# Optimization experiments

Measured on AMD Instinct MI355X. Metric: run time of the kernel, lower is better.

Reference implementation:

```python
import jax, jax.numpy as jnp
import numpy as np

N = 170000          # n_users + n_entities
NNZ = 2720000       # edges in sparse A_in (avg degree 16)
DIMS = [64, 64, 32, 16]
NEG_SLOPE = 0.01    # nn.LeakyReLU default
EPS = 1e-12         # F.normalize eps


def setup_inputs() -> dict:
    key = jax.random.key(0)
    ks = jax.random.split(key, 20)
    inp = {
        "embeddings": jax.random.normal(ks[0], (N, DIMS[0]), jnp.float32) * 0.1,
        "a_vals": jax.random.uniform(ks[1], (NNZ,), jnp.float32) / 16.0,  # ~row-normalized
    }
    # bi-interaction layer params, stored (in, out) so y = x @ W + b
    i = 2
    for l in range(3):
        din, dout = DIMS[l], DIMS[l + 1]
        s = 1.0 / np.sqrt(din)
        inp[f"w1_{l}"] = jax.random.normal(ks[i], (din, dout), jnp.float32) * s; i += 1
        inp[f"b1_{l}"] = jnp.zeros((dout,), jnp.float32)
        inp[f"w2_{l}"] = jax.random.normal(ks[i], (din, dout), jnp.float32) * s; i += 1
        inp[f"b2_{l}"] = jnp.zeros((dout,), jnp.float32)
    inp["a_rows"] = jax.random.randint(ks[i], (NNZ,), 0, N, jnp.int32); i += 1
    inp["a_cols"] = jax.random.randint(ks[i], (NNZ,), 0, N, jnp.int32)
    return inp


def _leaky(x):
    return jnp.where(x >= 0, x, NEG_SLOPE * x)


def _l2norm(x):
    n = jnp.sqrt(jnp.sum(x * x, axis=1, keepdims=True))
    return x / jnp.maximum(n, EPS)


def _spmm(vals, rows, cols, emb):
    # sparse A (COO) @ emb : gather source rows, scale, scatter-add to dest rows
    msgs = vals[:, None] * emb[cols]          # (nnz, d)
    return jax.ops.segment_sum(msgs, rows, num_segments=N)


def reference(embeddings, a_vals,
              w1_0, b1_0, w2_0, b2_0,
              w1_1, b1_1, w2_1, b2_1,
              w1_2, b1_2, w2_2, b2_2,
              a_rows, a_cols):
    layers = [(w1_0, b1_0, w2_0, b2_0),
              (w1_1, b1_1, w2_1, b2_1),
              (w1_2, b1_2, w2_2, b2_2)]
    ego = embeddings
    all_embed = [ego]
    for (w1, b1, w2, b2) in layers:
        side = _spmm(a_vals, a_rows, a_cols, ego)            # (N, d_in)
        sum_e = _leaky((ego + side) @ w1 + b1)               # bi-interaction
        bi_e = _leaky((ego * side) @ w2 + b2)
        ego = sum_e + bi_e                                   # dropout = identity (eval)
        all_embed.append(_l2norm(ego))
    return jnp.concatenate(all_embed, axis=1)                # (N, 176)
```

## Files before the change

### kernel.cpp

```cpp
#include <hip/hip_runtime.h>
#include <hip/hip_bf16.h>

#define NEG_SLOPE 0.01f
#define L2EPS 1e-12f
#define SCAN_CHUNK 2048
#define PART_CH 8192
#define BSHIFT 9

__device__ __forceinline__ unsigned short f2bf(float f) {
    unsigned u = __float_as_uint(f);
    return (unsigned short)((u + 0x7fffu + ((u >> 16) & 1u)) >> 16);
}


__global__ void scan_sum(const int* __restrict__ counts, int* __restrict__ partials, int n) {
    __shared__ int red[256];
    int base = blockIdx.x * SCAN_CHUNK;
    int s = 0;
    for (int i = threadIdx.x; i < SCAN_CHUNK; i += 256) {
        int idx = base + i;
        s += (idx < n) ? counts[idx] : 0;
    }
    red[threadIdx.x] = s; __syncthreads();
    for (int o = 128; o > 0; o >>= 1) {
        if (threadIdx.x < o) red[threadIdx.x] += red[threadIdx.x + o];
        __syncthreads();
    }
    if (threadIdx.x == 0) partials[blockIdx.x] = red[0];
}

__global__ void scan_partials(int* __restrict__ partials, int nb, int* __restrict__ out, int n) {
    if (threadIdx.x == 0 && blockIdx.x == 0) {
        int run = 0;
        for (int i = 0; i < nb; i++) { int v = partials[i]; partials[i] = run; run += v; }
        out[n] = run;
    }
}

__global__ void scan_apply(const int* __restrict__ counts, const int* __restrict__ partials,
                           int* __restrict__ out, int n) {
    __shared__ int lsum[256];
    int base = blockIdx.x * SCAN_CHUNK;
    int t = threadIdx.x;
    int my[8];
    int s = 0;
    int tb = base + t * 8;
    for (int i = 0; i < 8; i++) { int idx = tb + i; int v = (idx < n) ? counts[idx] : 0; my[i] = v; s += v; }
    lsum[t] = s; __syncthreads();
    for (int o = 1; o < 256; o <<= 1) {
        int v = (t >= o) ? lsum[t - o] : 0;
        __syncthreads();
        lsum[t] += v;
        __syncthreads();
    }
    int excl = lsum[t] - s + partials[blockIdx.x];
    for (int i = 0; i < 8; i++) {
        int idx = tb + i;
        if (idx < n) { out[idx] = excl; excl += my[i]; }
    }
}


__global__ void part_hist(const int* __restrict__ rows, int* __restrict__ hist,
                          int nnz, int nchunks, int B) {
    __shared__ int h[512];
    int c = blockIdx.x;
    for (int i = threadIdx.x; i < B; i += 256) h[i] = 0;
    __syncthreads();
    int s = c * PART_CH, e = min(s + PART_CH, nnz);
    for (int i = s + threadIdx.x; i < e; i += 256) atomicAdd(&h[rows[i] >> BSHIFT], 1);
    __syncthreads();
    for (int b = threadIdx.x; b < B; b += 256) hist[b * nchunks + c] = h[b];
}

__global__ void part_scatter(const int* __restrict__ rows, const int* __restrict__ cols,
                             const float* __restrict__ vals, const int* __restrict__ hscan,
                             int2* __restrict__ tmp, int nnz, int nchunks, int B) {
    __shared__ int cur[512];
    int c = blockIdx.x;
    for (int b = threadIdx.x; b < B; b += 256) cur[b] = hscan[b * nchunks + c];
    __syncthreads();
    int s = c * PART_CH, e = min(s + PART_CH, nnz);
    for (int i = s + threadIdx.x; i < e; i += 256) {
        int r = rows[i];
        int p = atomicAdd(&cur[r >> BSHIFT], 1);
        unsigned u14 = __float2uint_rn(vals[i] * 262144.0f);
        if (u14 > 16383u) u14 = 16383u;
        tmp[p] = make_int2(((r & 511) << 18) | cols[i], (int)u14);
    }
}

__global__ void bucket_scatter(const int* __restrict__ hscan, const int2* __restrict__ tmp,
                               unsigned* __restrict__ pedge, int* __restrict__ offsets,
                               int nnz, int nchunks, int B, int n) {
    __shared__ int cnt[512];
    __shared__ int scn[256];
    int b = blockIdx.x;
    int t = threadIdx.x;
    int rbase = b << BSHIFT;
    cnt[t] = 0; cnt[t + 256] = 0;
    __syncthreads();
    int s = hscan[b * nchunks];
    int e = (b == B - 1) ? nnz : hscan[(b + 1) * nchunks];
    for (int j = s + t; j < e; j += 256) atomicAdd(&cnt[((unsigned)tmp[j].x) >> 18], 1);
    __syncthreads();
    int c0 = cnt[2 * t], c1 = cnt[2 * t + 1];
    int ssum = c0 + c1;
    scn[t] = ssum;
    __syncthreads();
    for (int o = 1; o < 256; o <<= 1) {
        int v = (t >= o) ? scn[t - o] : 0;
        __syncthreads();
        scn[t] += v;
        __syncthreads();
    }
    int excl = scn[t] - ssum + s;
    int g0 = rbase + 2 * t, g1 = g0 + 1;
    if (g0 < n) offsets[g0] = excl;
    if (g1 < n) offsets[g1] = excl + c0;
    cnt[2 * t] = excl;
    cnt[2 * t + 1] = excl + c0;
    if (b == B - 1 && t == 0) offsets[n] = nnz;
    __syncthreads();
    for (int j = s + t; j < e; j += 256) {
        int2 tt = tmp[j];
        int r9 = ((unsigned)tt.x) >> 18;
        int p = atomicAdd(&cnt[r9], 1);
        pedge[p] = (unsigned)(tt.x & 0x3FFFF) | ((unsigned)tt.y << 18);
    }
}


__global__ void embed_prep(const float* __restrict__ emb, unsigned short* __restrict__ egob,
                           float* __restrict__ outp, int nrows) {
    int idx = blockIdx.x * blockDim.x + threadIdx.x;
    if (idx >= nrows * 16) return;
    int row = idx >> 4, c = idx & 15;
    float4 v = ((const float4*)emb)[idx];
    ((float4*)(outp + (size_t)row * 176))[c] = v;
    ushort4 o;
    o.x = f2bf(v.x); o.y = f2bf(v.y); o.z = f2bf(v.z); o.w = f2bf(v.w);
    ((ushort4*)egob)[idx] = o;
}


__device__ __forceinline__ float leaky1(float x) { return x >= 0.f ? x : NEG_SLOPE * x; }

__device__ __forceinline__ void fma8(float v, uint4 qv, float* acc) {
    acc[0] += v * __uint_as_float(qv.x << 16);
    acc[1] += v * __uint_as_float(qv.x & 0xffff0000u);
    acc[2] += v * __uint_as_float(qv.y << 16);
    acc[3] += v * __uint_as_float(qv.y & 0xffff0000u);
    acc[4] += v * __uint_as_float(qv.z << 16);
    acc[5] += v * __uint_as_float(qv.z & 0xffff0000u);
    acc[6] += v * __uint_as_float(qv.w << 16);
    acc[7] += v * __uint_as_float(qv.w & 0xffff0000u);
}

__device__ __forceinline__ void unpack8(uint4 qv, float* e) {
    e[0] = __uint_as_float(qv.x << 16); e[1] = __uint_as_float(qv.x & 0xffff0000u);
    e[2] = __uint_as_float(qv.y << 16); e[3] = __uint_as_float(qv.y & 0xffff0000u);
    e[4] = __uint_as_float(qv.z << 16); e[5] = __uint_as_float(qv.z & 0xffff0000u);
    e[6] = __uint_as_float(qv.w << 16); e[7] = __uint_as_float(qv.w & 0xffff0000u);
}

#define V14 3.814697265625e-06f

template <int DIN, int DOUT>
__global__ __launch_bounds__(256, 4)
void fused_layer(const unsigned short* __restrict__ egob, const int* __restrict__ offs,
                 const unsigned* __restrict__ pedge,
                 const float* __restrict__ w1, const float* __restrict__ b1,
                 const float* __restrict__ w2, const float* __restrict__ b2,
                 unsigned short* __restrict__ egob_next,
                 float* __restrict__ outp, int col_off, int nrows) {
    constexpr int RPB = 64;
    constexpr int CPL = DIN / 4;
    constexpr int U4  = CPL / 8;
    constexpr int TX  = DOUT / 4;
    constexpr int TY  = 256 / TX;
    constexpr int RPT = RPB / TY;

    __shared__ float sU[DIN][RPB];
    __shared__ float sV[DIN][RPB];

    int tid = threadIdx.x;
    int row0 = blockIdx.x * RPB;

    if (tid < 64) {
        int g = row0 + tid;
        unsigned deg = (g < nrows) ? (unsigned)(offs[g + 1] - offs[g]) : 0u;
        unsigned key = (deg << 6) | (unsigned)tid;
#pragma unroll
        for (int size = 2; size <= 64; size <<= 1) {
#pragma unroll
            for (int stride = size >> 1; stride > 0; stride >>= 1) {
                unsigned other = __shfl_xor(key, stride, 64);
                bool dir = ((tid & size) == 0);
                bool lower = ((tid & stride) == 0);
                bool takeMin = (lower == dir);
                key = takeMin ? (key < other ? key : other) : (key > other ? key : other);
            }
        }
        ((int*)sU)[tid] = (int)(key & 63u);
    }
    __syncthreads();
    int r = tid >> 2, q = tid & 3;
    int pr = ((int*)sU)[r];
    __syncthreads();

    {
        int g = row0 + pr;
        float acc[CPL];
#pragma unroll
        for (int i = 0; i < CPL; i++) acc[i] = 0.f;
        if (g < nrows) {
            int j0 = offs[g], j1 = offs[g + 1];
            uint4 eq[U4];
            const uint4* ep = (const uint4*)(egob + (size_t)g * DIN) + q * U4;
#pragma unroll
            for (int u = 0; u < U4; u++) eq[u] = ep[u];

            int j = j0;
            unsigned ed[4];
            bool have = (j + 4 <= j1);
            if (have) {
#pragma unroll
                for (int m = 0; m < 4; m++) ed[m] = pedge[j + m];
            }
            while (have) {
                uint4 t[4][U4];
#pragma unroll
                for (int m = 0; m < 4; m++) {
                    const uint4* s = (const uint4*)(egob + (size_t)(ed[m] & 0x3FFFFu) * DIN) + q * U4;
#pragma unroll
                    for (int u = 0; u < U4; u++) t[m][u] = s[u];
                }
                bool nxt = (j + 8 <= j1);
                unsigned ed2[4];
                if (nxt) {
#pragma unroll
                    for (int m = 0; m < 4; m++) ed2[m] = pedge[j + 4 + m];
                }
#pragma unroll
                for (int m = 0; m < 4; m++) {
                    float v = (float)(ed[m] >> 18) * V14;
#pragma unroll
                    for (int u = 0; u < U4; u++) fma8(v, t[m][u], acc + u * 8);
                }
#pragma unroll
                for (int m = 0; m < 4; m++) ed[m] = ed2[m];
                j += 4;
                have = nxt;
            }
            for (; j < j1; ++j) {
                unsigned e0 = pedge[j];
                float v0 = (float)(e0 >> 18) * V14;
                const uint4* s0 = (const uint4*)(egob + (size_t)(e0 & 0x3FFFFu) * DIN) + q * U4;
                uint4 qa[U4];
#pragma unroll
                for (int u = 0; u < U4; u++) qa[u] = s0[u];
#pragma unroll
                for (int u = 0; u < U4; u++) fma8(v0, qa[u], acc + u * 8);
            }
#pragma unroll
            for (int u = 0; u < U4; u++) {
                float ev[8];
                unpack8(eq[u], ev);
                int k0 = q * CPL + u * 8;
#pragma unroll
                for (int z = 0; z < 8; z++) {
                    float e = ev[z], a = acc[u * 8 + z];
                    sU[k0 + z][pr] = e + a;
                    sV[k0 + z][pr] = e * a;
                }
            }
        } else {
#pragma unroll
            for (int i = 0; i < CPL; i++) { sU[q * CPL + i][pr] = 0.f; sV[q * CPL + i][pr] = 0.f; }
        }
    }
    __syncthreads();

    int tx = tid % TX, ty = tid / TX;
    float4 a1[RPT], a2[RPT];
#pragma unroll
    for (int i = 0; i < RPT; i++) {
        a1[i] = make_float4(0.f, 0.f, 0.f, 0.f);
        a2[i] = make_float4(0.f, 0.f, 0.f, 0.f);
    }

#pragma unroll 8
    for (int k = 0; k < DIN; k++) {
        float4 w1v = ((const float4*)w1)[k * TX + tx];
        float4 w2v = ((const float4*)w2)[k * TX + tx];
        float uv[RPT], vv[RPT];
        if constexpr (RPT == 4) {
            float4 t1 = *(const float4*)&sU[k][ty * 4];
            float4 t2 = *(const float4*)&sV[k][ty * 4];
            uv[0] = t1.x; uv[1] = t1.y; uv[2] = t1.z; uv[3] = t1.w;
            vv[0] = t2.x; vv[1] = t2.y; vv[2] = t2.z; vv[3] = t2.w;
        } else if constexpr (RPT == 2) {
            float2 t1 = *(const float2*)&sU[k][ty * 2];
            float2 t2 = *(const float2*)&sV[k][ty * 2];
            uv[0] = t1.x; uv[1] = t1.y;
            vv[0] = t2.x; vv[1] = t2.y;
        } else {
            uv[0] = sU[k][ty];
            vv[0] = sV[k][ty];
        }
#pragma unroll
        for (int i = 0; i < RPT; i++) {
            a1[i].x += uv[i] * w1v.x; a1[i].y += uv[i] * w1v.y; a1[i].z += uv[i] * w1v.z; a1[i].w += uv[i] * w1v.w;
            a2[i].x += vv[i] * w2v.x; a2[i].y += vv[i] * w2v.y; a2[i].z += vv[i] * w2v.z; a2[i].w += vv[i] * w2v.w;
        }
    }

    float4 bb1 = ((const float4*)b1)[tx];
    float4 bb2 = ((const float4*)b2)[tx];
#pragma unroll
    for (int i = 0; i < RPT; i++) {
        int g = row0 + ty * RPT + i;
        float4 x;
        x.x = leaky1(a1[i].x + bb1.x) + leaky1(a2[i].x + bb2.x);
        x.y = leaky1(a1[i].y + bb1.y) + leaky1(a2[i].y + bb2.y);
        x.z = leaky1(a1[i].z + bb1.z) + leaky1(a2[i].z + bb2.z);
        x.w = leaky1(a1[i].w + bb1.w) + leaky1(a2[i].w + bb2.w);
        float ss = x.x * x.x + x.y * x.y + x.z * x.z + x.w * x.w;
#pragma unroll
        for (int o = TX >> 1; o > 0; o >>= 1) ss += __shfl_xor(ss, o, 64);
        if (g < nrows) {
            if (egob_next) {
                ushort4 xb;
                xb.x = f2bf(x.x); xb.y = f2bf(x.y); xb.z = f2bf(x.z); xb.w = f2bf(x.w);
                ((ushort4*)(egob_next + (size_t)g * DOUT))[tx] = xb;
            }
            float inv = 1.f / fmaxf(sqrtf(ss), L2EPS);
            float4 y = make_float4(x.x * inv, x.y * inv, x.z * inv, x.w * inv);
            ((float4*)(outp + (size_t)g * 176 + col_off))[tx] = y;
        }
    }
}

extern "C" void kernel_launch(void* const* d_in, const int* in_sizes, int n_in,
                              void* d_out, int out_size, void* d_ws, size_t ws_size,
                              hipStream_t stream) {
    const float* emb   = (const float*)d_in[0];
    const float* avals = (const float*)d_in[1];
    const float* w1_0 = (const float*)d_in[2];  const float* b1_0 = (const float*)d_in[3];
    const float* w2_0 = (const float*)d_in[4];  const float* b2_0 = (const float*)d_in[5];
    const float* w1_1 = (const float*)d_in[6];  const float* b1_1 = (const float*)d_in[7];
    const float* w2_1 = (const float*)d_in[8];  const float* b2_1 = (const float*)d_in[9];
    const float* w1_2 = (const float*)d_in[10]; const float* b1_2 = (const float*)d_in[11];
    const float* w2_2 = (const float*)d_in[12]; const float* b2_2 = (const float*)d_in[13];
    const int* arows = (const int*)d_in[14];
    const int* acols = (const int*)d_in[15];
    float* outp = (float*)d_out;

    const int N   = in_sizes[0] / 64;
    const int NNZ = in_sizes[14];

    const int B       = (N + 511) >> BSHIFT;
    const int nchunks = (NNZ + PART_CH - 1) / PART_CH;
    const int NH      = B * nchunks;

    char* w = (char*)d_ws;
    size_t off = 0;
    auto carve = [&](size_t bytes) { char* p = w + off; off += (bytes + 255) & ~(size_t)255; return p; };
    int*   offsets  = (int*)  carve((size_t)(N + 1) * 4);
    int*   partials = (int*)  carve(1024);
    int*   hist     = (int*)  carve((size_t)(NH + 1) * 4);
    int*   hscan    = (int*)  carve((size_t)(NH + 1) * 4);
    unsigned* pedge = (unsigned*)carve((size_t)NNZ * 4);
    int2*  tmp      = (int2*) carve((size_t)NNZ * 8);
    unsigned short* egobA = (unsigned short*)carve((size_t)N * 64 * 2);
    unsigned short* egobB = (unsigned short*)carve((size_t)N * 64 * 2);

    const int NB2 = (NH + SCAN_CHUNK - 1) / SCAN_CHUNK;

    part_hist<<<nchunks, 256, 0, stream>>>(arows, hist, NNZ, nchunks, B);
    scan_sum<<<NB2, 256, 0, stream>>>(hist, partials, NH);
    scan_partials<<<1, 64, 0, stream>>>(partials, NB2, hscan, NH);
    scan_apply<<<NB2, 256, 0, stream>>>(hist, partials, hscan, NH);
    part_scatter<<<nchunks, 256, 0, stream>>>(arows, acols, avals, hscan, tmp, NNZ, nchunks, B);
    bucket_scatter<<<B, 256, 0, stream>>>(hscan, tmp, pedge, offsets, NNZ, nchunks, B, N);

    embed_prep<<<(N * 16 + 255) / 256, 256, 0, stream>>>(emb, egobA, outp, N);

    const int DB = (N + 63) / 64;

    fused_layer<64, 64><<<DB, 256, 0, stream>>>(egobA, offsets, pedge,
                                                w1_0, b1_0, w2_0, b2_0,
                                                egobB, outp, 64, N);
    fused_layer<64, 32><<<DB, 256, 0, stream>>>(egobB, offsets, pedge,
                                                w1_1, b1_1, w2_1, b2_1,
                                                egobA, outp, 128, N);
    fused_layer<32, 16><<<DB, 256, 0, stream>>>(egobA, offsets, pedge,
                                                w1_2, b1_2, w2_2, b2_2,
                                                nullptr, outp, 160, N);
}
```

Baseline: 582.4 us.

## Sort edges by column sub-bucket, use nontemporal output stores, raise occupancy

Within each row, the bucket scatter now also orders edges by the top bits of the column index (16 column sub-bins per row, 8192 LDS counters). This makes gathers from neighbouring rows touch nearby source rows, which should improve cache locality in the SpMM. Output stores in embed_prep and fused_layer switch to nontemporal stores so the write-once output does not pollute the cache. The launch bounds minimum-block hint rises from 4 to 5, which may force register spills, and the larger LDS histogram with per-thread 32-entry scans adds cost to the sort kernel.

```diff
diff --git a/kernel.cpp b/kernel.cpp
--- a/kernel.cpp
+++ b/kernel.cpp
@@ -10,6 +10,12 @@
 __device__ __forceinline__ unsigned short f2bf(float f) {
     unsigned u = __float_as_uint(f);
     return (unsigned short)((u + 0x7fffu + ((u >> 16) & 1u)) >> 16);
+}
+
+typedef float f32x4 __attribute__((ext_vector_type(4)));
+__device__ __forceinline__ void nt_store_f4(float4 v, float* p) {
+    f32x4 x; x.x = v.x; x.y = v.y; x.z = v.z; x.w = v.w;
+    __builtin_nontemporal_store(x, (f32x4*)p);
 }
 
 
@@ -93,19 +99,26 @@
 __global__ void bucket_scatter(const int* __restrict__ hscan, const int2* __restrict__ tmp,
                                unsigned* __restrict__ pedge, int* __restrict__ offsets,
                                int nnz, int nchunks, int B, int n) {
-    __shared__ int cnt[512];
+    __shared__ int cnt[8192];
     __shared__ int scn[256];
     int b = blockIdx.x;
     int t = threadIdx.x;
     int rbase = b << BSHIFT;
-    cnt[t] = 0; cnt[t + 256] = 0;
+    for (int i = t; i < 8192; i += 256) cnt[i] = 0;
     __syncthreads();
     int s = hscan[b * nchunks];
     int e = (b == B - 1) ? nnz : hscan[(b + 1) * nchunks];
-    for (int j = s + t; j < e; j += 256) atomicAdd(&cnt[((unsigned)tmp[j].x) >> 18], 1);
-    __syncthreads();
-    int c0 = cnt[2 * t], c1 = cnt[2 * t + 1];
-    int ssum = c0 + c1;
+    for (int j = s + t; j < e; j += 256) {
+        unsigned x = (unsigned)tmp[j].x;
+        unsigned bin = ((x >> 18) << 4) | ((x & 0x3FFFFu) >> 14);
+        atomicAdd(&cnt[bin], 1);
+    }
+    __syncthreads();
+    int base = t * 32;
+    int vals[32];
+    int ssum = 0;
+#pragma unroll
+    for (int i = 0; i < 32; i++) { vals[i] = cnt[base + i]; ssum += vals[i]; }
     scn[t] = ssum;
     __syncthreads();
     for (int o = 1; o < 256; o <<= 1) {
@@ -115,18 +128,23 @@
         __syncthreads();
     }
     int excl = scn[t] - ssum + s;
-    int g0 = rbase + 2 * t, g1 = g0 + 1;
-    if (g0 < n) offsets[g0] = excl;
-    if (g1 < n) offsets[g1] = excl + c0;
-    cnt[2 * t] = excl;
-    cnt[2 * t + 1] = excl + c0;
-    if (b == B - 1 && t == 0) offsets[n] = nnz;
+#pragma unroll
+    for (int i = 0; i < 32; i++) { cnt[base + i] = excl; excl += vals[i]; }
+    __syncthreads();
+    {
+        int r0 = 2 * t, r1 = r0 + 1;
+        int g0 = rbase + r0, g1 = rbase + r1;
+        if (g0 < n) offsets[g0] = cnt[r0 << 4];
+        if (g1 < n) offsets[g1] = cnt[r1 << 4];
+        if (b == B - 1 && t == 0) offsets[n] = nnz;
+    }
     __syncthreads();
     for (int j = s + t; j < e; j += 256) {
         int2 tt = tmp[j];
-        int r9 = ((unsigned)tt.x) >> 18;
-        int p = atomicAdd(&cnt[r9], 1);
-        pedge[p] = (unsigned)(tt.x & 0x3FFFF) | ((unsigned)tt.y << 18);
+        unsigned x = (unsigned)tt.x;
+        unsigned bin = ((x >> 18) << 4) | ((x & 0x3FFFFu) >> 14);
+        int p = atomicAdd(&cnt[bin], 1);
+        pedge[p] = (x & 0x3FFFFu) | ((unsigned)tt.y << 18);
     }
 }
 
@@ -137,7 +155,7 @@
     if (idx >= nrows * 16) return;
     int row = idx >> 4, c = idx & 15;
     float4 v = ((const float4*)emb)[idx];
-    ((float4*)(outp + (size_t)row * 176))[c] = v;
+    nt_store_f4(v, outp + (size_t)row * 176 + c * 4);
     ushort4 o;
     o.x = f2bf(v.x); o.y = f2bf(v.y); o.z = f2bf(v.z); o.w = f2bf(v.w);
     ((ushort4*)egob)[idx] = o;
@@ -167,7 +185,7 @@
 #define V14 3.814697265625e-06f
 
 template <int DIN, int DOUT>
-__global__ __launch_bounds__(256, 4)
+__global__ __launch_bounds__(256, 5)
 void fused_layer(const unsigned short* __restrict__ egob, const int* __restrict__ offs,
                  const unsigned* __restrict__ pedge,
                  const float* __restrict__ w1, const float* __restrict__ b1,
@@ -337,7 +355,7 @@
             }
             float inv = 1.f / fmaxf(sqrtf(ss), L2EPS);
             float4 y = make_float4(x.x * inv, x.y * inv, x.z * inv, x.w * inv);
-            ((float4*)(outp + (size_t)g * 176 + col_off))[tx] = y;
+            nt_store_f4(y, outp + (size_t)g * 176 + col_off + tx * 4);
         }
     }
 }
```

Measured after the change: 610.0 us. 4.8% more time.
